# Performance work log

Hardware: AMD Instinct MI355X
Metric: run time of the kernel (lower is better)

The kernel has to match this reference:

```python
import jax, jax.numpy as jnp
import numpy as np

N = 50000
E = 800000
IN = 128
HID = 320
HEADS = 4
D = HID // HEADS  # 80
EPS = 1e-5
NEG_SLOPE = 0.2


def sage_conv(x, src, dst, wl, bl, wr, n):
    # PyG SAGEConv (mean aggr): out = lin_l(mean_j x_j) + lin_r(x_i)
    msg = x[src]                                               # [E, HID]
    s = jax.ops.segment_sum(msg, dst, num_segments=n)          # [N, HID]
    cnt = jax.ops.segment_sum(jnp.ones((src.shape[0], 1), x.dtype), dst, num_segments=n)
    mean = s / jnp.maximum(cnt, 1.0)
    return mean @ wl + bl + x @ wr


def gat_conv(x, src, dst, w, a_src, a_dst, b, n):
    # PyG GATConv with add_self_loops=True, concat=True
    loop = jnp.arange(n, dtype=src.dtype)
    src = jnp.concatenate([src, loop])
    dst = jnp.concatenate([dst, loop])
    xh = (x @ w).reshape(n, HEADS, D)                          # [N, H, D]
    al = jnp.sum(xh * a_src, axis=-1)                          # [N, H] (source term)
    ar = jnp.sum(xh * a_dst, axis=-1)                          # [N, H] (target term)
    e = jax.nn.leaky_relu(al[src] + ar[dst], NEG_SLOPE)        # [E', H]
    m = jax.ops.segment_max(e, dst, num_segments=n)            # [N, H]
    m = jnp.where(jnp.isfinite(m), m, 0.0)
    ex = jnp.exp(e - m[dst])                                   # [E', H]
    den = jax.ops.segment_sum(ex, dst, num_segments=n)         # [N, H]
    num = jax.ops.segment_sum(ex[:, :, None] * xh[src], dst, num_segments=n)  # [N, H, D]
    out = num / jnp.maximum(den, 1e-16)[:, :, None]
    return out.reshape(n, HEADS * D) + b


def batch_norm(x, gamma, beta):
    # eval-mode BN with running_mean=0, running_var=1
    return x * (gamma / jnp.sqrt(1.0 + EPS)) + beta


def setup_inputs() -> dict:
    key = jax.random.key(0)
    ks = jax.random.split(key, 24)
    s = 0.05
    inp = {
        'x': jax.random.normal(ks[0], (N, IN), jnp.float32),
        'edge_index': jax.random.randint(ks[1], (2, E), 0, N, jnp.int32),
        'w_in': jax.random.normal(ks[2], (IN, HID), jnp.float32) * s,
        'b_in': jnp.zeros((HID,), jnp.float32),
        'sage0_wl': jax.random.normal(ks[3], (HID, HID), jnp.float32) * s,
        'sage0_bl': jnp.zeros((HID,), jnp.float32),
        'sage0_wr': jax.random.normal(ks[4], (HID, HID), jnp.float32) * s,
        'gat1_w': jax.random.normal(ks[5], (HID, HID), jnp.float32) * s,
        'gat1_asrc': jax.random.normal(ks[6], (HEADS, D), jnp.float32) * s,
        'gat1_adst': jax.random.normal(ks[7], (HEADS, D), jnp.float32) * s,
        'gat1_b': jnp.zeros((HID,), jnp.float32),
        'sage2_wl': jax.random.normal(ks[8], (HID, HID), jnp.float32) * s,
        'sage2_bl': jnp.zeros((HID,), jnp.float32),
        'sage2_wr': jax.random.normal(ks[9], (HID, HID), jnp.float32) * s,
        'gat3_w': jax.random.normal(ks[10], (HID, HID), jnp.float32) * s,
        'gat3_asrc': jax.random.normal(ks[11], (HEADS, D), jnp.float32) * s,
        'gat3_adst': jax.random.normal(ks[12], (HEADS, D), jnp.float32) * s,
        'gat3_b': jnp.zeros((HID,), jnp.float32),
        'bn_gamma': jnp.ones((4, HID), jnp.float32),
        'bn_beta': jnp.zeros((4, HID), jnp.float32),
        'cls_w1': jax.random.normal(ks[13], (HID, HID // 2), jnp.float32) * s,
        'cls_b1': jnp.zeros((HID // 2,), jnp.float32),
        'cls_w2': jax.random.normal(ks[14], (HID // 2, 2), jnp.float32) * s,
        'cls_b2': jnp.zeros((2,), jnp.float32),
    }
    return inp


def reference(x, edge_index, w_in, b_in,
              sage0_wl, sage0_bl, sage0_wr,
              gat1_w, gat1_asrc, gat1_adst, gat1_b,
              sage2_wl, sage2_bl, sage2_wr,
              gat3_w, gat3_asrc, gat3_adst, gat3_b,
              bn_gamma, bn_beta,
              cls_w1, cls_b1, cls_w2, cls_b2):
    src, dst = edge_index[0], edge_index[1]
    h = jax.nn.relu(x @ w_in + b_in)  # dropout is identity in eval
    # layer 0: SAGE
    h = sage_conv(h, src, dst, sage0_wl, sage0_bl, sage0_wr, N)
    h = jax.nn.relu(batch_norm(h, bn_gamma[0], bn_beta[0]))
    # layer 1: GAT
    h = gat_conv(h, src, dst, gat1_w, gat1_asrc, gat1_adst, gat1_b, N)
    h = jax.nn.relu(batch_norm(h, bn_gamma[1], bn_beta[1]))
    # layer 2: SAGE
    h = sage_conv(h, src, dst, sage2_wl, sage2_bl, sage2_wr, N)
    h = jax.nn.relu(batch_norm(h, bn_gamma[2], bn_beta[2]))
    # layer 3: GAT
    h = gat_conv(h, src, dst, gat3_w, gat3_asrc, gat3_adst, gat3_b, N)
    h = jax.nn.relu(batch_norm(h, bn_gamma[3], bn_beta[3]))
    embeddings = h
    out = jax.nn.relu(h @ cls_w1 + cls_b1) @ cls_w2 + cls_b2
    return (out, embeddings)
```

## Files before the change

### kernel.cpp

```cpp
#include <hip/hip_runtime.h>
#include <cstdint>

#define MN 50000
#define EN 800000
#define HID 320
#define HEADS 4
#define HDIM 80
#define NEG_SLOPE 0.2f

typedef __attribute__((ext_vector_type(4))) float f32x4;
typedef __attribute__((ext_vector_type(8))) short short8v;

__device__ __forceinline__ unsigned short f2bf(float f){
  unsigned u = __float_as_uint(f);
  return (unsigned short)((u + 0x7fffu + ((u >> 16) & 1u)) >> 16);
}
__device__ __forceinline__ float bf2f(unsigned short s){
  return __uint_as_float(((unsigned)s) << 16);
}
__device__ __forceinline__ void gldlds16(const void* g, void* l){
  __builtin_amdgcn_global_load_lds((const __attribute__((address_space(1))) void*)g,
                                   (__attribute__((address_space(3))) void*)l, 16, 0, 0);
}

__global__ void hist_kernel(const int* __restrict__ dst, int* __restrict__ hist, int E) {
  int e = blockIdx.x * 256 + threadIdx.x;
  if (e < E) atomicAdd(&hist[dst[e]], 1);
}

__global__ __launch_bounds__(1024) void scan_kernel(const int* __restrict__ hist,
                                                    int* __restrict__ row_off, int n) {
  __shared__ int part[1024];
  int t = threadIdx.x;
  int chunk = (n + 1023) >> 10;
  int beg = t * chunk, end = beg + chunk;
  if (end > n) end = n;
  if (beg > n) beg = n;
  int s = 0;
  for (int i = beg; i < end; i++) s += hist[i];
  part[t] = s;
  __syncthreads();
  for (int off = 1; off < 1024; off <<= 1) {
    int v = (t >= off) ? part[t - off] : 0;
    __syncthreads();
    if (t >= off) part[t] += v;
    __syncthreads();
  }
  int run = (t > 0) ? part[t - 1] : 0;
  for (int i = beg; i < end; i++) { row_off[i] = run; run += hist[i]; }
  if (t == 0) row_off[n] = part[1023];
}

__global__ void scatter_kernel(const int* __restrict__ src, const int* __restrict__ dst,
                               const int* __restrict__ row_off, int* __restrict__ cur,
                               int* __restrict__ csr_src, int E) {
  int e = blockIdx.x * 256 + threadIdx.x;
  if (e < E) {
    int d = dst[e];
    int p = atomicAdd(&cur[d], 1);
    csr_src[row_off[d] + p] = src[e];
  }
}

__global__ void wprep(const float* __restrict__ W, unsigned short* __restrict__ dst,
                      int K, int Nsz, int total) {
  int idx = blockIdx.x * 256 + threadIdx.x;
  if (idx >= total) return;
  int j = idx & 7;
  int c1 = (idx >> 3) & 3;
  int rest = idx >> 5;
  int col = rest % Nsz;
  int kt = rest / Nsz;
  int chunk = c1 ^ ((col >> 1) & 3);
  int kp = kt * 32 + chunk * 8 + j;
  int seg = kp / K;
  int k = kp - seg * K;
  float v = W[(size_t)k * Nsz + col];
  unsigned short h = f2bf(v);
  unsigned short o = (seg == 2) ? f2bf(v - bf2f(h)) : h;
  dst[(size_t)kt * Nsz * 32 + (size_t)col * 32 + c1 * 8 + j] = o;
}

template<int CW, bool SRCF32, int SEGT, int NPASS, int MODE>
__global__ __launch_bounds__(128 * CW, 4) void mfma_gemm(
    const char* __restrict__ A1, const char* __restrict__ A2,
    const char* __restrict__ Wq,
    const float* __restrict__ bias, const float* __restrict__ gamma,
    const float* __restrict__ beta, void* __restrict__ outp, int M)
{
  static_assert(!SRCF32 || CW == 4, "");
  constexpr int TPB = 128 * CW;
  constexpr int N = CW * 80;
  constexpr int NT = NPASS * 3 * SEGT;
  constexpr int TILEB = N * 64;
  constexpr int AIT = (384 + TPB - 1) / TPB;
  __shared__ __align__(16) char ldsA[2 * 7680];
  __shared__ __align__(16) char ldsB[2 * TILEB];
  const int tid = threadIdx.x;
  const int lane = tid & 63;
  const int w = tid >> 6;
  const int rw = w & 1, cwv = w >> 1;
  const int bm = blockIdx.x * 96;
  const int kc = (lane >> 4) & 3;
  const int l15 = lane & 15;

  int aoff[3], boff[5];
  #pragma unroll
  for (int fr = 0; fr < 3; fr++) aoff[fr] = (rw * 48 + fr * 16 + l15) * 80 + kc * 16;
  #pragma unroll
  for (int cf = 0; cf < 5; cf++) {
    int col = cwv * 80 + cf * 16 + l15;
    boff[cf] = col * 64 + ((kc ^ ((col >> 1) & 3)) << 4);
  }

  f32x4 acc[3][5];
  #pragma unroll
  for (int i = 0; i < 3; i++)
    #pragma unroll
    for (int j = 0; j < 5; j++) { f32x4 z = {0.f, 0.f, 0.f, 0.f}; acc[i][j] = z; }

  f32x4 areg[AIT][2];
  auto issueA = [&](int t) -> bool {
    int pass = 0, tt = t;
    if constexpr (NPASS == 2) { pass = t / (3 * SEGT); tt = t - pass * (3 * SEGT); }
    int seg = tt / SEGT;
    int kk = tt - seg * SEGT;
    const char* __restrict__ base = pass ? A2 : A1;
    #pragma unroll
    for (int it = 0; it < AIT; it++) {
      int s = tid + it * TPB;
      if (s < 384) {
        int row = s >> 2, c = s & 3;
        int r = bm + row; if (r >= M) r = M - 1;
        if constexpr (SRCF32) {
          const char* p = base + (size_t)r * 512 + kk * 128 + c * 32;
          areg[it][0] = *(const f32x4*)p;
          areg[it][1] = *(const f32x4*)(p + 16);
        } else {
          const char* p = base + (size_t)r * 1280 + (seg == 1 ? 640 : 0) + kk * 64 + c * 16;
          areg[it][0] = *(const f32x4*)p;
        }
      }
    }
    return seg == 1;
  };
  auto writeA = [&](int buf, bool lo) {
    #pragma unroll
    for (int it = 0; it < AIT; it++) {
      int s = tid + it * TPB;
      if (s < 384) {
        int row = s >> 2, c = s & 3;
        char* d = &ldsA[buf * 7680 + row * 80 + c * 16];
        if constexpr (SRCF32) {
          short8v v;
          #pragma unroll
          for (int j = 0; j < 8; j++) {
            float f = (j < 4) ? areg[it][0][j] : areg[it][1][j - 4];
            unsigned short h = f2bf(f);
            unsigned short o = lo ? f2bf(f - bf2f(h)) : h;
            v[j] = (short)o;
          }
          *(short8v*)d = v;
        } else {
          f32x4 t4 = areg[it][0];
          *(short8v*)d = *(short8v*)&t4;
        }
      }
    }
  };
  auto issueB = [&](int t, int buf) {
    const char* __restrict__ src = Wq + (size_t)t * TILEB;
    for (int s = tid; s < N * 4; s += TPB)
      gldlds16(src + (size_t)s * 16, &ldsB[buf * TILEB + s * 16]);
  };

  bool plo = issueA(0);
  issueB(0, 0);
  writeA(0, plo);
  __syncthreads();

  for (int t = 0; t < NT; ++t) {
    int curb = t & 1, nxt = curb ^ 1;
    bool lo = false;
    if (t + 1 < NT) { lo = issueA(t + 1); issueB(t + 1, nxt); }
    short8v af0 = *(const short8v*)&ldsA[curb * 7680 + aoff[0]];
    short8v af1 = *(const short8v*)&ldsA[curb * 7680 + aoff[1]];
    short8v af2 = *(const short8v*)&ldsA[curb * 7680 + aoff[2]];
    #pragma unroll
    for (int cf = 0; cf < 5; cf++) {
      short8v bv = *(const short8v*)&ldsB[curb * TILEB + boff[cf]];
      acc[0][cf] = __builtin_amdgcn_mfma_f32_16x16x32_bf16(af0, bv, acc[0][cf], 0, 0, 0);
      acc[1][cf] = __builtin_amdgcn_mfma_f32_16x16x32_bf16(af1, bv, acc[1][cf], 0, 0, 0);
      acc[2][cf] = __builtin_amdgcn_mfma_f32_16x16x32_bf16(af2, bv, acc[2][cf], 0, 0, 0);
    }
    if (t + 1 < NT) writeA(nxt, lo);
    __syncthreads();
  }

  const float bnrs = 0.99999500003749971f;
  #pragma unroll
  for (int fr = 0; fr < 3; fr++) {
    int rbase = bm + rw * 48 + fr * 16 + (lane >> 4) * 4;
    #pragma unroll
    for (int cf = 0; cf < 5; cf++) {
      int col = cwv * 80 + cf * 16 + l15;
      float bi = 0.f, sc = 1.f, be = 0.f;
      if constexpr (MODE >= 1) bi = bias[col];
      if constexpr (MODE == 3) { sc = gamma[col] * bnrs; be = beta[col]; }
      #pragma unroll
      for (int rg = 0; rg < 4; rg++) {
        int r = rbase + rg;
        if (r < M) {
          float v = acc[fr][cf][rg];
          if constexpr (MODE >= 1) v += bi;
          if constexpr (MODE == 3) v = v * sc + be;
          if constexpr (MODE >= 1) v = v > 0.f ? v : 0.f;
          if constexpr (MODE >= 2) {
            unsigned short h = f2bf(v);
            unsigned short g = f2bf(v - bf2f(h));
            unsigned short* o = (unsigned short*)outp;
            o[(size_t)r * 640 + col] = h;
            o[(size_t)r * 640 + 320 + col] = g;
          } else {
            ((float*)outp)[(size_t)r * N + col] = v;
          }
        }
      }
    }
  }
}

__global__ __launch_bounds__(256) void sage_agg_split(const unsigned* __restrict__ hp,
    const int* __restrict__ row_off, const int* __restrict__ csr_src,
    unsigned* __restrict__ outp, int n) {
  int node = blockIdx.x * 8 + (threadIdx.x >> 5);
  int lane = threadIdx.x & 31;
  if (node >= n) return;
  int beg = row_off[node], end = row_off[node + 1];
  float s0[5] = {0,0,0,0,0}, s1[5] = {0,0,0,0,0};
  float t0[5] = {0,0,0,0,0}, t1[5] = {0,0,0,0,0};
  for (int e = beg; e < end; e++) {
    const unsigned* row = hp + (size_t)csr_src[e] * 320;
    #pragma unroll
    for (int k = 0; k < 5; k++) {
      unsigned dh = row[lane + 32 * k];
      unsigned dl = row[160 + lane + 32 * k];
      s0[k] += bf2f((unsigned short)dh);
      s1[k] += bf2f((unsigned short)(dh >> 16));
      t0[k] += bf2f((unsigned short)dl);
      t1[k] += bf2f((unsigned short)(dl >> 16));
    }
  }
  int deg = end - beg;
  float inv = 1.0f / (float)(deg > 0 ? deg : 1);
  unsigned* orow = outp + (size_t)node * 320;
  #pragma unroll
  for (int k = 0; k < 5; k++) {
    float v0 = (s0[k] + t0[k]) * inv;
    float v1 = (s1[k] + t1[k]) * inv;
    unsigned short h0 = f2bf(v0), h1 = f2bf(v1);
    unsigned short g0 = f2bf(v0 - bf2f(h0)), g1 = f2bf(v1 - bf2f(h1));
    orow[lane + 32 * k] = (unsigned)h0 | ((unsigned)h1 << 16);
    orow[160 + lane + 32 * k] = (unsigned)g0 | ((unsigned)g1 << 16);
  }
}

__global__ void gat_prep(const float* __restrict__ xh,
    const float* __restrict__ asrc, const float* __restrict__ adst,
    float* __restrict__ al, float* __restrict__ ar, int n) {
  int idx = blockIdx.x * 256 + threadIdx.x;
  if (idx >= n * HEADS) return;
  int node = idx >> 2, hh = idx & 3;
  const float* row = xh + (size_t)node * HID + hh * HDIM;
  const float* as = asrc + hh * HDIM;
  const float* ad = adst + hh * HDIM;
  float sl = 0.f, sr = 0.f;
  for (int d = 0; d < HDIM; d++) { float v = row[d]; sl += v * as[d]; sr += v * ad[d]; }
  al[idx] = sl;
  ar[idx] = sr;
}

template<bool F32OUT>
__global__ __launch_bounds__(256) void gat_agg(const float* __restrict__ xh,
    const int* __restrict__ row_off, const int* __restrict__ csr_src,
    const float* __restrict__ al, const float* __restrict__ ar,
    const float* __restrict__ bias, const float* __restrict__ gamma,
    const float* __restrict__ beta, unsigned short* __restrict__ outS,
    float* __restrict__ outF, int n) {
  int node = (blockIdx.x << 2) + (threadIdx.x >> 6);
  int lane = threadIdx.x & 63;
  if (node >= n) return;
  int beg = row_off[node], end = row_off[node + 1];
  float arv[4], alv_i[4];
  #pragma unroll
  for (int hh = 0; hh < 4; hh++) { arv[hh] = ar[node * 4 + hh]; alv_i[hh] = al[node * 4 + hh]; }
  float m[4];
  #pragma unroll
  for (int hh = 0; hh < 4; hh++) {
    float v = alv_i[hh] + arv[hh];
    m[hh] = v > 0.f ? v : NEG_SLOPE * v;
  }
  for (int e = beg + lane; e < end; e += 64) {
    int s = csr_src[e];
    #pragma unroll
    for (int hh = 0; hh < 4; hh++) {
      float v = al[s * 4 + hh] + arv[hh];
      v = v > 0.f ? v : NEG_SLOPE * v;
      m[hh] = fmaxf(m[hh], v);
    }
  }
  #pragma unroll
  for (int off = 1; off < 64; off <<= 1) {
    #pragma unroll
    for (int hh = 0; hh < 4; hh++) m[hh] = fmaxf(m[hh], __shfl_xor(m[hh], off));
  }
  float den[4] = {0.f, 0.f, 0.f, 0.f};
  float num[5] = {0.f, 0.f, 0.f, 0.f, 0.f};
  int pos[5], hk[5];
  #pragma unroll
  for (int k = 0; k < 5; k++) { pos[k] = lane + (k << 6); hk[k] = pos[k] / HDIM; }
  for (int e = beg - 1; e < end; e++) {
    int s = (e < beg) ? node : csr_src[e];
    float ex[4];
    #pragma unroll
    for (int hh = 0; hh < 4; hh++) {
      float v = al[s * 4 + hh] + arv[hh];
      v = v > 0.f ? v : NEG_SLOPE * v;
      ex[hh] = expf(v - m[hh]);
      den[hh] += ex[hh];
    }
    const float* row = xh + (size_t)s * HID;
    #pragma unroll
    for (int k = 0; k < 5; k++) num[k] += ex[hk[k]] * row[pos[k]];
  }
  const float bnrs = 0.99999500003749971f;
  #pragma unroll
  for (int k = 0; k < 5; k++) {
    int p = pos[k];
    float d = den[hk[k]];
    d = d > 1e-16f ? d : 1e-16f;
    float v = num[k] / d + bias[p];
    v = v * (gamma[p] * bnrs) + beta[p];
    v = v > 0.f ? v : 0.f;
    unsigned short h = f2bf(v);
    outS[(size_t)node * 640 + p] = h;
    outS[(size_t)node * 640 + 320 + p] = f2bf(v - bf2f(h));
    if constexpr (F32OUT) outF[(size_t)node * 320 + p] = v;
  }
}

__global__ void cls2_kernel(const float* __restrict__ tbuf, const float* __restrict__ w2,
                            const float* __restrict__ b2, float* __restrict__ out, int M) {
  int r = blockIdx.x * 256 + threadIdx.x;
  if (r >= M) return;
  const float* row = tbuf + (size_t)r * 160;
  float a0 = b2[0], a1 = b2[1];
  for (int d = 0; d < 160; d++) {
    float v = row[d];
    a0 += v * w2[2 * d];
    a1 += v * w2[2 * d + 1];
  }
  out[2 * r] = a0;
  out[2 * r + 1] = a1;
}

extern "C" void kernel_launch(void* const* d_in, const int* in_sizes, int n_in,
                              void* d_out, int out_size, void* d_ws, size_t ws_size,
                              hipStream_t stream) {
  const float* x    = (const float*)d_in[0];
  const int*   ei   = (const int*)d_in[1];
  const float* w_in = (const float*)d_in[2];
  const float* b_in = (const float*)d_in[3];
  const float* s0wl = (const float*)d_in[4];
  const float* s0bl = (const float*)d_in[5];
  const float* s0wr = (const float*)d_in[6];
  const float* g1w  = (const float*)d_in[7];
  const float* g1as = (const float*)d_in[8];
  const float* g1ad = (const float*)d_in[9];
  const float* g1b  = (const float*)d_in[10];
  const float* s2wl = (const float*)d_in[11];
  const float* s2bl = (const float*)d_in[12];
  const float* s2wr = (const float*)d_in[13];
  const float* g3w  = (const float*)d_in[14];
  const float* g3as = (const float*)d_in[15];
  const float* g3ad = (const float*)d_in[16];
  const float* g3b  = (const float*)d_in[17];
  const float* bng  = (const float*)d_in[18];
  const float* bnb  = (const float*)d_in[19];
  const float* cw1  = (const float*)d_in[20];
  const float* cb1  = (const float*)d_in[21];
  const float* cw2  = (const float*)d_in[22];
  const float* cb2  = (const float*)d_in[23];

  char* ws = (char*)d_ws;
  size_t off = 0;
  auto alloc = [&](size_t b) {
    void* p = (void*)(ws + off);
    off += (b + 255) & ~(size_t)255;
    return p;
  };
  const size_t SB = (size_t)MN * 1280;
  char* S0 = (char*)alloc(SB);
  char* S1 = (char*)alloc(SB);
  char* S2 = (char*)alloc(SB);
  char* WQ = (char*)alloc(4239360);
  float* al      = (float*)alloc((size_t)MN * HEADS * 4);
  float* ar      = (float*)alloc((size_t)MN * HEADS * 4);
  int*   row_off = (int*)alloc((size_t)(MN + 1) * 4);
  int*   hist    = (int*)alloc((size_t)MN * 4);
  int*   curw    = (int*)alloc((size_t)MN * 4);
  int*   csr     = (int*)alloc((size_t)EN * 4);

  float* outp = (float*)d_out;
  float* emb  = outp + (size_t)MN * 2;

  const int* srcp = ei;
  const int* dstp = ei + EN;

  hipMemsetAsync(hist, 0, MN * 4, stream);
  hipMemsetAsync(curw, 0, MN * 4, stream);
  hist_kernel<<<(EN + 255) / 256, 256, 0, stream>>>(dstp, hist, EN);
  scan_kernel<<<1, 1024, 0, stream>>>(hist, row_off, MN);
  scatter_kernel<<<(EN + 255) / 256, 256, 0, stream>>>(srcp, dstp, row_off, curw, csr, EN);

  char* wq_in = WQ + 0;
  char* wq_s0 = WQ + 245760;
  char* wq_g1 = WQ + 1474560;
  char* wq_s2 = WQ + 2088960;
  char* wq_g3 = WQ + 3317760;
  char* wq_cl = WQ + 3932160;
  int tot = 12 * 320 * 32;
  wprep<<<(tot + 255) / 256, 256, 0, stream>>>(w_in, (unsigned short*)wq_in, 128, 320, tot);
  tot = 30 * 320 * 32;
  wprep<<<(tot + 255) / 256, 256, 0, stream>>>(s0wl, (unsigned short*)wq_s0, 320, 320, tot);
  wprep<<<(tot + 255) / 256, 256, 0, stream>>>(s0wr, (unsigned short*)(wq_s0 + 614400), 320, 320, tot);
  wprep<<<(tot + 255) / 256, 256, 0, stream>>>(g1w,  (unsigned short*)wq_g1, 320, 320, tot);
  wprep<<<(tot + 255) / 256, 256, 0, stream>>>(s2wl, (unsigned short*)wq_s2, 320, 320, tot);
  wprep<<<(tot + 255) / 256, 256, 0, stream>>>(s2wr, (unsigned short*)(wq_s2 + 614400), 320, 320, tot);
  wprep<<<(tot + 255) / 256, 256, 0, stream>>>(g3w,  (unsigned short*)wq_g3, 320, 320, tot);
  tot = 30 * 160 * 32;
  wprep<<<(tot + 255) / 256, 256, 0, stream>>>(cw1, (unsigned short*)wq_cl, 320, 160, tot);

  const int gx = (MN + 95) / 96;
  const int ga = (MN + 3) / 4;
  const int gs = (MN + 7) / 8;

  mfma_gemm<4, true, 4, 1, 2><<<gx, 512, 0, stream>>>(
      (const char*)x, nullptr, wq_in, b_in, nullptr, nullptr, S0, MN);
  sage_agg_split<<<gs, 256, 0, stream>>>((const unsigned*)S0, row_off, csr, (unsigned*)S1, MN);
  mfma_gemm<4, false, 10, 2, 3><<<gx, 512, 0, stream>>>(
      S1, S0, wq_s0, s0bl, bng, bnb, S2, MN);
  mfma_gemm<4, false, 10, 1, 0><<<gx, 512, 0, stream>>>(
      S2, nullptr, wq_g1, nullptr, nullptr, nullptr, emb, MN);
  gat_prep<<<(MN * HEADS + 255) / 256, 256, 0, stream>>>(emb, g1as, g1ad, al, ar, MN);
  gat_agg<false><<<ga, 256, 0, stream>>>(
      emb, row_off, csr, al, ar, g1b, bng + 320, bnb + 320, (unsigned short*)S0, nullptr, MN);
  sage_agg_split<<<gs, 256, 0, stream>>>((const unsigned*)S0, row_off, csr, (unsigned*)S1, MN);
  mfma_gemm<4, false, 10, 2, 3><<<gx, 512, 0, stream>>>(
      S1, S0, wq_s2, s2bl, bng + 640, bnb + 640, S2, MN);
  mfma_gemm<4, false, 10, 1, 0><<<gx, 512, 0, stream>>>(
      S2, nullptr, wq_g3, nullptr, nullptr, nullptr, S0, MN);
  gat_prep<<<(MN * HEADS + 255) / 256, 256, 0, stream>>>((const float*)S0, g3as, g3ad, al, ar, MN);
  gat_agg<true><<<ga, 256, 0, stream>>>(
      (const float*)S0, row_off, csr, al, ar, g3b, bng + 960, bnb + 960,
      (unsigned short*)S1, emb, MN);
  mfma_gemm<2, false, 10, 1, 1><<<gx, 256, 0, stream>>>(
      S1, nullptr, wq_cl, cb1, nullptr, nullptr, S2, MN);
  cls2_kernel<<<(MN + 255) / 256, 256, 0, stream>>>((const float*)S2, cw2, cb2, outp, MN);
}
```

Measured before the change: 1.540 ms.

## Drop GAT max pass by shifting softmax with self-loop score; vectorize small kernels

The GAT aggregation no longer makes a separate pass over each node's edges to find the softmax maximum. It shifts the exponentials by the node's own self-loop score, which also lets it start the numerator and denominator with the self term. Lanes are remapped so each 16-lane group handles one head, which removes the per-element head lookup, and the edge source index is made wave-uniform with readfirstlane. The fast __expf is used, and gat_prep and cls2 now use float4 loads with unrolled loops. The cost is numerical: exponentials can overflow if an edge score exceeds the self score by a large margin.

```diff
diff --git a/kernel.cpp b/kernel.cpp
--- a/kernel.cpp
+++ b/kernel.cpp
@@ -271,11 +271,16 @@
   int idx = blockIdx.x * 256 + threadIdx.x;
   if (idx >= n * HEADS) return;
   int node = idx >> 2, hh = idx & 3;
-  const float* row = xh + (size_t)node * HID + hh * HDIM;
-  const float* as = asrc + hh * HDIM;
-  const float* ad = adst + hh * HDIM;
+  const f32x4* row = (const f32x4*)(xh + (size_t)node * HID + hh * HDIM);
+  const f32x4* as = (const f32x4*)(asrc + hh * HDIM);
+  const f32x4* ad = (const f32x4*)(adst + hh * HDIM);
   float sl = 0.f, sr = 0.f;
-  for (int d = 0; d < HDIM; d++) { float v = row[d]; sl += v * as[d]; sr += v * ad[d]; }
+  #pragma unroll
+  for (int d = 0; d < 20; d++) {
+    f32x4 v = row[d], a = as[d], b = ad[d];
+    #pragma unroll
+    for (int j = 0; j < 4; j++) { sl += v[j] * a[j]; sr += v[j] * b[j]; }
+  }
   al[idx] = sl;
   ar[idx] = sr;
 }
@@ -291,60 +296,53 @@
   int lane = threadIdx.x & 63;
   if (node >= n) return;
   int beg = row_off[node], end = row_off[node + 1];
-  float arv[4], alv_i[4];
-  #pragma unroll
-  for (int hh = 0; hh < 4; hh++) { arv[hh] = ar[node * 4 + hh]; alv_i[hh] = al[node * 4 + hh]; }
-  float m[4];
-  #pragma unroll
-  for (int hh = 0; hh < 4; hh++) {
-    float v = alv_i[hh] + arv[hh];
-    m[hh] = v > 0.f ? v : NEG_SLOPE * v;
-  }
-  for (int e = beg + lane; e < end; e += 64) {
-    int s = csr_src[e];
-    #pragma unroll
-    for (int hh = 0; hh < 4; hh++) {
-      float v = al[s * 4 + hh] + arv[hh];
-      v = v > 0.f ? v : NEG_SLOPE * v;
-      m[hh] = fmaxf(m[hh], v);
-    }
-  }
-  #pragma unroll
-  for (int off = 1; off < 64; off <<= 1) {
-    #pragma unroll
-    for (int hh = 0; hh < 4; hh++) m[hh] = fmaxf(m[hh], __shfl_xor(m[hh], off));
-  }
-  float den[4] = {0.f, 0.f, 0.f, 0.f};
-  float num[5] = {0.f, 0.f, 0.f, 0.f, 0.f};
-  int pos[5], hk[5];
-  #pragma unroll
-  for (int k = 0; k < 5; k++) { pos[k] = lane + (k << 6); hk[k] = pos[k] / HDIM; }
-  for (int e = beg - 1; e < end; e++) {
-    int s = (e < beg) ? node : csr_src[e];
+  const int hh = lane >> 4;
+  const int posb = hh * 80 + (lane & 15);
+
+  float arv[4], sh[4];
+  f32x4 a4i = *(const f32x4*)(al + (size_t)node * 4);
+  #pragma unroll
+  for (int h = 0; h < 4; h++) {
+    arv[h] = ar[node * 4 + h];
+    float v = a4i[h] + arv[h];
+    sh[h] = fmaxf(v, NEG_SLOPE * v);
+  }
+  float den[4] = {1.f, 1.f, 1.f, 1.f};
+  const float* selfrow = xh + (size_t)node * HID;
+  float num[5];
+  #pragma unroll
+  for (int k = 0; k < 5; k++) num[k] = selfrow[posb + 16 * k];
+
+  for (int e = beg; e < end; e++) {
+    int s = __builtin_amdgcn_readfirstlane(csr_src[e]);
+    f32x4 a4 = *(const f32x4*)(al + (size_t)s * 4);
     float ex[4];
     #pragma unroll
-    for (int hh = 0; hh < 4; hh++) {
-      float v = al[s * 4 + hh] + arv[hh];
-      v = v > 0.f ? v : NEG_SLOPE * v;
-      ex[hh] = expf(v - m[hh]);
-      den[hh] += ex[hh];
-    }
-    const float* row = xh + (size_t)s * HID;
-    #pragma unroll
-    for (int k = 0; k < 5; k++) num[k] += ex[hk[k]] * row[pos[k]];
-  }
+    for (int h = 0; h < 4; h++) {
+      float v = a4[h] + arv[h];
+      v = fmaxf(v, NEG_SLOPE * v);
+      float r = __expf(v - sh[h]);
+      ex[h] = r;
+      den[h] += r;
+    }
+    float exsel = hh < 2 ? (hh == 0 ? ex[0] : ex[1]) : (hh == 2 ? ex[2] : ex[3]);
+    const float* __restrict__ row = xh + (size_t)s * HID;
+    #pragma unroll
+    for (int k = 0; k < 5; k++) num[k] += exsel * row[posb + 16 * k];
+  }
+
+  float dsel = hh < 2 ? (hh == 0 ? den[0] : den[1]) : (hh == 2 ? den[2] : den[3]);
+  float dinv = 1.0f / dsel;
   const float bnrs = 0.99999500003749971f;
   #pragma unroll
   for (int k = 0; k < 5; k++) {
-    int p = pos[k];
-    float d = den[hk[k]];
-    d = d > 1e-16f ? d : 1e-16f;
-    float v = num[k] / d + bias[p];
+    int p = posb + 16 * k;
+    float v = num[k] * dinv + bias[p];
     v = v * (gamma[p] * bnrs) + beta[p];
-    v = v > 0.f ? v : 0.f;
-    unsigned short h = f2bf(v);
-    outS[(size_t)node * 640 + p] = h;
-    outS[(size_t)node * 640 + 320 + p] = f2bf(v - bf2f(h));
+    v = fmaxf(v, 0.f);
+    unsigned short h2 = f2bf(v);
+    outS[(size_t)node * 640 + p] = h2;
+    outS[(size_t)node * 640 + 320 + p] = f2bf(v - bf2f(h2));
     if constexpr (F32OUT) outF[(size_t)node * 320 + p] = v;
   }
 }
@@ -353,12 +351,17 @@
                             const float* __restrict__ b2, float* __restrict__ out, int M) {
   int r = blockIdx.x * 256 + threadIdx.x;
   if (r >= M) return;
-  const float* row = tbuf + (size_t)r * 160;
+  const f32x4* row = (const f32x4*)(tbuf + (size_t)r * 160);
   float a0 = b2[0], a1 = b2[1];
-  for (int d = 0; d < 160; d++) {
-    float v = row[d];
-    a0 += v * w2[2 * d];
-    a1 += v * w2[2 * d + 1];
+  #pragma unroll
+  for (int d4 = 0; d4 < 40; d4++) {
+    f32x4 v = row[d4];
+    #pragma unroll
+    for (int j = 0; j < 4; j++) {
+      int d = d4 * 4 + j;
+      a0 += v[j] * w2[2 * d];
+      a1 += v[j] * w2[2 * d + 1];
+    }
   }
   out[2 * r] = a0;
   out[2 * r + 1] = a1;
```

Measured after the change: 1.501 ms. 1.03x faster.
